# Performance work log

Measured on AMD Instinct MI355X. Metric: run time of the kernel, lower is better.

Reference implementation:

```python
import jax, jax.numpy as jnp
import numpy as np

N_NODES = 100_000
N_EDGES = 1_600_000
VOCAB = 10_000
NUM_GRAPHS = 512
D_EMB, D_HID, D_OUT = 64, 128, 64


def _sage_conv(h, src, dst, Wl, b, Wr, num_nodes):
    """PyG SAGEConv with mean aggregation: lin_l(mean_{j in N(i)} x_j) + lin_r(x_i)."""
    msgs = h[src]                                               # [E, D]
    agg = jax.ops.segment_sum(msgs, dst, num_segments=num_nodes)
    deg = jax.ops.segment_sum(jnp.ones((src.shape[0], 1), h.dtype), dst,
                              num_segments=num_nodes)
    agg = agg / jnp.maximum(deg, 1.0)                           # mean over neighbors
    return agg @ Wl + b + h @ Wr


def setup_inputs() -> dict:
    key = jax.random.key(0)
    ks = jax.random.split(key, 12)
    x = jax.random.randint(ks[0], (N_NODES,), 0, VOCAB)
    edge_index = jax.random.randint(ks[1], (2, N_EDGES), 0, N_NODES)
    batch = jnp.sort(jax.random.randint(ks[2], (N_NODES,), 0, NUM_GRAPHS))
    edge_attr = jax.random.uniform(ks[3], (N_EDGES, 1), dtype=jnp.float32)
    embed = jax.random.normal(ks[4], (VOCAB, D_EMB), dtype=jnp.float32) * 0.02
    W1l = jax.random.normal(ks[5], (D_EMB, D_HID), dtype=jnp.float32) / np.sqrt(D_EMB)
    b1 = jnp.zeros((D_HID,), jnp.float32)
    W1r = jax.random.normal(ks[6], (D_EMB, D_HID), dtype=jnp.float32) / np.sqrt(D_EMB)
    W2l = jax.random.normal(ks[7], (D_HID, D_OUT), dtype=jnp.float32) / np.sqrt(D_HID)
    b2 = jnp.zeros((D_OUT,), jnp.float32)
    W2r = jax.random.normal(ks[8], (D_HID, D_OUT), dtype=jnp.float32) / np.sqrt(D_HID)
    return {"x": x, "edge_index": edge_index, "batch": batch, "edge_attr": edge_attr,
            "embed": embed, "W1l": W1l, "b1": b1, "W1r": W1r,
            "W2l": W2l, "b2": b2, "W2r": W2r}


def reference(x, edge_index, batch, edge_attr, embed, W1l, b1, W1r, W2l, b2, W2r):
    # edge_attr is passed in the original forward but PyG SAGEConv ignores edge weights.
    src, dst = edge_index[0], edge_index[1]
    h = embed[x]                                                # [N, 64]
    h = jax.nn.relu(_sage_conv(h, src, dst, W1l, b1, W1r, N_NODES))  # [N, 128]
    h = _sage_conv(h, src, dst, W2l, b2, W2r, N_NODES)          # [N, 64]
    out = jax.ops.segment_max(h, batch, num_segments=NUM_GRAPHS)  # [G, 64]
    return out
```

## Files before the change

### kernel.cpp

```cpp
#include <hip/hip_runtime.h>
#include <cstdint>

#define NN 100000
#define NE 1600000
#define NG 512
#define NP 100032
#define VOCAB 10000
#define NBUK 64
#define BSZ 1563
#define CAP 28672
#define TILE 2048

typedef unsigned short u16;
typedef u16      u16x8  __attribute__((ext_vector_type(8)));
typedef __bf16   bf16x8 __attribute__((ext_vector_type(8)));
typedef float    f32x4  __attribute__((ext_vector_type(4)));
typedef unsigned uint4v __attribute__((ext_vector_type(4)));

__device__ __forceinline__ u16 f2bf(float f) {
    unsigned u = __float_as_uint(f);
    unsigned r = ((u >> 16) & 1u) + 0x7FFFu;
    return (u16)((u + r) >> 16);
}
__device__ __forceinline__ float bf2f(u16 h) {
    return __uint_as_float(((unsigned)h) << 16);
}

__device__ __forceinline__ unsigned encF(float f) {
    unsigned s = __float_as_uint(f);
    return (s & 0x80000000u) ? ~s : (s | 0x80000000u);
}
__device__ __forceinline__ float decF(unsigned m) {
    unsigned s = (m & 0x80000000u) ? (m ^ 0x80000000u) : ~m;
    return __uint_as_float(s);
}

template <bool HI>
__device__ __forceinline__ void gather8(const int* __restrict__ csr, int beg, int end,
                                        const u16* __restrict__ table, int lane,
                                        float acc[8]) {
    const int sub = lane >> 3, g8 = (lane & 7) * 8;
    for (int base = beg; base < end; base += 64) {
        int n = min(64, end - base);
        int s = (lane < n) ? csr[base + lane] : 0;
        for (int c = 0; c * 8 < n; c += 2) {
            int i0 = c * 8 + sub;
            int e0 = __shfl(s, i0, 64);
            int r0 = HI ? (e0 >> 17) : (e0 & 0x1FFFF);
            u16x8 v0 = *(const u16x8*)(table + (size_t)r0 * 64 + g8);
            bool m1 = (c + 1) * 8 < n;
            int i1 = (c + 1) * 8 + sub;
            int e1 = __shfl(s, m1 ? i1 : 0, 64);
            int r1 = HI ? (e1 >> 17) : (e1 & 0x1FFFF);
            u16x8 v1 = *(const u16x8*)(table + (size_t)r1 * 64 + g8);
            unsigned k0 = (i0 < n) ? 0xFFFFFFFFu : 0u;
            unsigned k1 = (m1 && i1 < n) ? 0xFFFFFFFFu : 0u;
            uint4v u0 = __builtin_bit_cast(uint4v, v0);
            uint4v u1 = __builtin_bit_cast(uint4v, v1);
            #pragma unroll
            for (int k = 0; k < 4; ++k) {
                unsigned a = u0[k] & k0, b = u1[k] & k1;
                acc[2 * k]     += __uint_as_float(a << 16);
                acc[2 * k + 1] += __uint_as_float(a & 0xFFFF0000u);
                acc[2 * k]     += __uint_as_float(b << 16);
                acc[2 * k + 1] += __uint_as_float(b & 0xFFFF0000u);
            }
        }
    }
}

__device__ __forceinline__ float reduce_dim(const float acc[8], float* sT, int lane) {
    const int sub = lane >> 3, g8 = (lane & 7) * 8;
    #pragma unroll
    for (int j = 0; j < 8; ++j) sT[sub * 64 + g8 + j] = acc[j];
    float t = 0.0f;
    #pragma unroll
    for (int sg = 0; sg < 8; ++sg) t += sT[sg * 64 + lane];
    return t;
}

__device__ __forceinline__ void prepW_body(const float* __restrict__ Wa,
                                           const float* __restrict__ Wb,
                                           int mode, u16* __restrict__ Wpk, int idx) {
    int fid = idx >> 6, lane = idx & 63;
    int cT = fid >> 2, ks = fid & 3;
    int quad = lane >> 4, l16 = lane & 15;
    int n = cT * 16 + l16;
    u16x8 v;
    #pragma unroll
    for (int j = 0; j < 8; ++j) {
        int k = ks * 32 + quad * 8 + j;
        float f = (mode == 0) ? (k < 64 ? Wa[k * 128 + n] : Wb[(k - 64) * 128 + n])
                              : (n < 64 ? Wa[k * 64 + n] : Wb[k * 64 + (n - 64)]);
        v[j] = f2bf(f);
    }
    *(u16x8*)(Wpk + idx * 8) = v;
}

__global__ __launch_bounds__(256) void k_prep(
        const float* __restrict__ emb, u16* __restrict__ embB,
        const float* __restrict__ W1l, const float* __restrict__ W1r,
        u16* __restrict__ Wpk1,
        const float* __restrict__ W2l, const float* __restrict__ W2r,
        u16* __restrict__ Wpk2, unsigned* __restrict__ om) {
    int bid = blockIdx.x, t = threadIdx.x;
    if (bid < 2500) {
        int i = bid * 256 + t;
        if (i < VOCAB * 64) embB[i] = f2bf(emb[i]);
    } else if (bid < 2508) {
        prepW_body(W1l, W1r, 0, Wpk1, (bid - 2500) * 256 + t);
    } else if (bid < 2516) {
        prepW_body(W2l, W2r, 1, Wpk2, (bid - 2508) * 256 + t);
    } else {
        int i = (bid - 2516) * 256 + t;
        if (i < NG * 64) om[i] = 0x007FFFFFu;
    }
}

__global__ __launch_bounds__(256) void k_bucket(const int* __restrict__ ei,
                                                int* __restrict__ gcur,
                                                unsigned* __restrict__ gbuf) {
    __shared__ int cnt[NBUK];
    __shared__ int start[NBUK];
    __shared__ int gbase[NBUK];
    __shared__ unsigned buf[TILE];
    __shared__ unsigned char bkt[TILE];
    const int t = threadIdx.x;
    const int e0 = blockIdx.x * (NE / 256);
    const int e1 = e0 + (NE / 256);
    for (int tb = e0; tb < e1; tb += TILE) {
        const int tc = min(TILE, e1 - tb);
        if (t < NBUK) cnt[t] = 0;
        __syncthreads();
        unsigned ent[TILE / 256];
        unsigned char eb[TILE / 256];
        u16 rk[TILE / 256];
        int nm = 0;
        for (int i = t; i < tc; i += 256) {
            int dst = ei[NE + tb + i];
            int src = ei[tb + i];
            unsigned b = (unsigned)dst / BSZ;
            unsigned dl = (unsigned)dst - b * BSZ;
            ent[nm] = (dl << 17) | (unsigned)src;
            eb[nm] = (unsigned char)b;
            rk[nm] = (u16)atomicAdd(&cnt[b], 1);
            ++nm;
        }
        __syncthreads();
        if (t < 64) {
            int c = cnt[t];
            int s = c;
            #pragma unroll
            for (int d = 1; d < 64; d <<= 1) {
                int v = __shfl_up(s, d, 64);
                if (t >= d) s += v;
            }
            start[t] = s - c;
            gbase[t] = atomicAdd(&gcur[t], c);
        }
        __syncthreads();
        for (int k = 0; k < nm; ++k) {
            int pos = start[eb[k]] + rk[k];
            buf[pos] = ent[k];
            bkt[pos] = eb[k];
        }
        __syncthreads();
        for (int i = t; i < tc; i += 256) {
            unsigned b = bkt[i];
            gbuf[(size_t)b * CAP + gbase[b] + (i - start[b])] = buf[i];
        }
        __syncthreads();
    }
}

__global__ __launch_bounds__(1024) void k_csr(const unsigned* __restrict__ gbuf,
                                              const int* __restrict__ gcur,
                                              const int* __restrict__ x,
                                              int* __restrict__ off,
                                              int* __restrict__ csr) {
    __shared__ int hist[BSZ];
    __shared__ int curL[BSZ];
    __shared__ int sc[1024];
    __shared__ int sb[64];
    const int b = blockIdx.x, t = threadIdx.x;
    for (int i = t; i < BSZ; i += 1024) hist[i] = 0;
    if (t < 64) sb[t] = (t < b) ? gcur[t] : 0;
    __syncthreads();
    const int size = gcur[b];
    const unsigned* gb = gbuf + (size_t)b * CAP;
    for (int i = t; i < size; i += 1024)
        atomicAdd(&hist[gb[i] >> 17], 1);
    for (int d = 32; d > 0; d >>= 1) {
        if (t < d) sb[t] += sb[t + d];
        __syncthreads();
    }
    const int gbase = sb[0];
    int a0 = (2 * t < BSZ) ? hist[2 * t] : 0;
    int a1 = (2 * t + 1 < BSZ) ? hist[2 * t + 1] : 0;
    sc[t] = a0 + a1;
    __syncthreads();
    for (int d = 1; d < 1024; d <<= 1) {
        int v = (t >= d) ? sc[t - d] : 0;
        __syncthreads();
        sc[t] += v;
        __syncthreads();
    }
    int ex = (t == 0) ? 0 : sc[t - 1];
    if (2 * t < BSZ) hist[2 * t] = ex;
    if (2 * t + 1 < BSZ) hist[2 * t + 1] = ex + a0;
    __syncthreads();
    const int g0 = b * BSZ;
    for (int i = t; i < BSZ; i += 1024) {
        int v = gbase + hist[i];
        curL[i] = v;
        if (g0 + i <= NN) off[g0 + i] = v;
    }
    __syncthreads();
    for (int i = t; i < size; i += 1024) {
        unsigned ent = gb[i];
        int src = (int)(ent & 0x1FFFFu);
        int dl  = (int)(ent >> 17);
        int pos = atomicAdd(&curL[dl], 1);
        csr[pos] = src | (x[src] << 17);
    }
}

__global__ __launch_bounds__(256) void k_gather1(const int* __restrict__ off,
                                                 const int* __restrict__ csr,
                                                 const int* __restrict__ x,
                                                 const u16* __restrict__ embB,
                                                 u16* __restrict__ A1) {
    __shared__ float sT[4][512];
    int wv = threadIdx.x >> 6, lane = threadIdx.x & 63;
    for (int grp = blockIdx.x; grp * 4 < NN; grp += gridDim.x) {
        int wid = grp * 4 + wv;
        int beg = off[wid], end = off[wid + 1];
        float acc[8] = {0.f, 0.f, 0.f, 0.f, 0.f, 0.f, 0.f, 0.f};
        gather8<true>(csr, beg, end, embB, lane, acc);
        float t = reduce_dim(acc, sT[wv], lane);
        A1[wid * 128 + lane] = f2bf(t / fmaxf((float)(end - beg), 1.0f));
        A1[wid * 128 + 64 + lane] = embB[x[wid] * 64 + lane];
    }
}

__global__ __launch_bounds__(256) void k_gemm12(
        const u16* __restrict__ A1, const u16* __restrict__ Wpk1,
        const u16* __restrict__ Wpk2, const float* __restrict__ b1,
        u16* __restrict__ P, u16* __restrict__ Q) {
    __shared__ __align__(16) u16 sH1[64][136];
    int w = threadIdx.x >> 6, lane = threadIdx.x & 63;
    int quad = lane >> 4, l16 = lane & 15;
    u16x8 bf1[2][4], bf2[2][4];
    #pragma unroll
    for (int ct = 0; ct < 2; ++ct)
        #pragma unroll
        for (int ks = 0; ks < 4; ++ks) {
            int fid = (w * 2 + ct) * 4 + ks;
            bf1[ct][ks] = *(const u16x8*)(Wpk1 + (fid * 64 + lane) * 8);
            bf2[ct][ks] = *(const u16x8*)(Wpk2 + (fid * 64 + lane) * 8);
        }
    int r0 = blockIdx.x * 64;
    #pragma unroll
    for (int rt = 0; rt < 4; ++rt) {
        int row = r0 + rt * 16 + l16;
        u16x8 a[4];
        #pragma unroll
        for (int ks = 0; ks < 4; ++ks)
            a[ks] = *(const u16x8*)(A1 + row * 128 + ks * 32 + quad * 8);
        #pragma unroll
        for (int ct = 0; ct < 2; ++ct) {
            f32x4 acc = {0.f, 0.f, 0.f, 0.f};
            #pragma unroll
            for (int ks = 0; ks < 4; ++ks)
                acc = __builtin_amdgcn_mfma_f32_16x16x32_bf16(
                    __builtin_bit_cast(bf16x8, a[ks]),
                    __builtin_bit_cast(bf16x8, bf1[ct][ks]), acc, 0, 0, 0);
            int col = w * 32 + ct * 16 + l16;
            float bias = b1[col];
            int lr = rt * 16 + quad * 4;
            #pragma unroll
            for (int reg = 0; reg < 4; ++reg)
                sH1[lr + reg][col] = f2bf(fmaxf(acc[reg] + bias, 0.f));
        }
    }
    __syncthreads();
    #pragma unroll
    for (int rt = 0; rt < 4; ++rt) {
        u16x8 a[4];
        #pragma unroll
        for (int ks = 0; ks < 4; ++ks)
            a[ks] = *(const u16x8*)(&sH1[rt * 16 + l16][ks * 32 + quad * 8]);
        #pragma unroll
        for (int ct = 0; ct < 2; ++ct) {
            f32x4 acc = {0.f, 0.f, 0.f, 0.f};
            #pragma unroll
            for (int ks = 0; ks < 4; ++ks)
                acc = __builtin_amdgcn_mfma_f32_16x16x32_bf16(
                    __builtin_bit_cast(bf16x8, a[ks]),
                    __builtin_bit_cast(bf16x8, bf2[ct][ks]), acc, 0, 0, 0);
            int col = w * 32 + ct * 16 + l16;
            int gr = r0 + rt * 16 + quad * 4;
            u16* dstT = (col < 64) ? P : Q;
            int c = col & 63;
            #pragma unroll
            for (int reg = 0; reg < 4; ++reg)
                dstT[(gr + reg) * 64 + c] = f2bf(acc[reg]);
        }
    }
}

__global__ __launch_bounds__(256) void k_final(const int* __restrict__ off,
                                               const int* __restrict__ csr,
                                               const u16* __restrict__ P,
                                               const u16* __restrict__ Q,
                                               const float* __restrict__ b2,
                                               const int* __restrict__ batch,
                                               unsigned* __restrict__ om) {
    __shared__ float sT[4][512];
    __shared__ float sR[4][64];
    __shared__ int sG[4];
    int wv = threadIdx.x >> 6, lane = threadIdx.x & 63;
    for (int grp = blockIdx.x; grp * 4 < NN; grp += gridDim.x) {
        int node = grp * 4 + wv;
        int beg = off[node], end = off[node + 1];
        float acc[8] = {0.f, 0.f, 0.f, 0.f, 0.f, 0.f, 0.f, 0.f};
        gather8<false>(csr, beg, end, P, lane, acc);
        float t = reduce_dim(acc, sT[wv], lane);
        float r = t / fmaxf((float)(end - beg), 1.0f) + b2[lane]
                + bf2f(Q[node * 64 + lane]);
        int g = batch[node];
        sR[wv][lane] = r;
        if (lane == 0) sG[wv] = g;
        __syncthreads();
        bool leader = (wv == 0) || (sG[wv - 1] != g);
        if (leader) {
            float m = r;
            for (int u = wv + 1; u < 4 && sG[u] == g; ++u) m = fmaxf(m, sR[u][lane]);
            atomicMax(&om[g * 64 + lane], encF(m));
        }
        __syncthreads();
    }
}

__global__ void k_decode(const unsigned* __restrict__ om, float* __restrict__ out) {
    int i = blockIdx.x * blockDim.x + threadIdx.x;
    if (i < NG * 64) out[i] = decF(om[i]);
}

extern "C" void kernel_launch(void* const* d_in, const int* in_sizes, int n_in,
                              void* d_out, int out_size, void* d_ws, size_t ws_size,
                              hipStream_t stream) {
    const int*   x     = (const int*)d_in[0];
    const int*   ei    = (const int*)d_in[1];
    const int*   batch = (const int*)d_in[2];
    const float* emb   = (const float*)d_in[4];
    const float* W1l   = (const float*)d_in[5];
    const float* b1    = (const float*)d_in[6];
    const float* W1r   = (const float*)d_in[7];
    const float* W2l   = (const float*)d_in[8];
    const float* b2    = (const float*)d_in[9];
    const float* W2r   = (const float*)d_in[10];
    float* out = (float*)d_out;

    char* p = (char*)d_ws;
    u16* A1   = (u16*)p;               p += (size_t)NP * 128 * 2;
    u16* P    = (u16*)p;               p += (size_t)NP * 64 * 2;
    u16* Q    = (u16*)p;               p += (size_t)NP * 64 * 2;
    int* csr  = (int*)p;               p += (size_t)NE * 4;
    unsigned* gbuf = (unsigned*)p;     p += (size_t)NBUK * CAP * 4;
    int* gcur = (int*)p;               p += NBUK * 4;
    int* off  = (int*)p;               p += (size_t)(NN + 1) * 4;
    u16* Wpk1 = (u16*)p;               p += 16384 * 2;
    u16* Wpk2 = (u16*)p;               p += 16384 * 2;
    u16* embB = (u16*)p;               p += (size_t)VOCAB * 64 * 2;
    unsigned* om = (unsigned*)p;

    hipMemsetAsync(gcur, 0, sizeof(int) * NBUK, stream);
    k_prep<<<2644, 256, 0, stream>>>(emb, embB, W1l, W1r, Wpk1, W2l, W2r, Wpk2, om);
    k_bucket<<<256, 256, 0, stream>>>(ei, gcur, gbuf);
    k_csr<<<NBUK, 1024, 0, stream>>>(gbuf, gcur, x, off, csr);
    k_gather1<<<2048, 256, 0, stream>>>(off, csr, x, embB, A1);
    k_gemm12<<<NP / 64, 256, 0, stream>>>(A1, Wpk1, Wpk2, b1, P, Q);
    k_final<<<2048, 256, 0, stream>>>(off, csr, P, Q, b2, batch, om);
    k_decode<<<(NG * 64 + 255) / 256, 256, 0, stream>>>(om, out);
}
```

Baseline: 253.2 us.

## Use 256 CSR buckets with wave-shuffle scans and deepen gather unroll

```diff
diff --git a/kernel.cpp b/kernel.cpp
--- a/kernel.cpp
+++ b/kernel.cpp
@@ -6,9 +6,9 @@
 #define NG 512
 #define NP 100032
 #define VOCAB 10000
-#define NBUK 64
-#define BSZ 1563
-#define CAP 28672
+#define NBUK 256
+#define BSZ 391
+#define CAP 7680
 #define TILE 2048
 
 typedef unsigned short u16;
@@ -43,27 +43,27 @@
     for (int base = beg; base < end; base += 64) {
         int n = min(64, end - base);
         int s = (lane < n) ? csr[base + lane] : 0;
-        for (int c = 0; c * 8 < n; c += 2) {
-            int i0 = c * 8 + sub;
-            int e0 = __shfl(s, i0, 64);
-            int r0 = HI ? (e0 >> 17) : (e0 & 0x1FFFF);
-            u16x8 v0 = *(const u16x8*)(table + (size_t)r0 * 64 + g8);
-            bool m1 = (c + 1) * 8 < n;
-            int i1 = (c + 1) * 8 + sub;
-            int e1 = __shfl(s, m1 ? i1 : 0, 64);
-            int r1 = HI ? (e1 >> 17) : (e1 & 0x1FFFF);
-            u16x8 v1 = *(const u16x8*)(table + (size_t)r1 * 64 + g8);
-            unsigned k0 = (i0 < n) ? 0xFFFFFFFFu : 0u;
-            unsigned k1 = (m1 && i1 < n) ? 0xFFFFFFFFu : 0u;
-            uint4v u0 = __builtin_bit_cast(uint4v, v0);
-            uint4v u1 = __builtin_bit_cast(uint4v, v1);
-            #pragma unroll
-            for (int k = 0; k < 4; ++k) {
-                unsigned a = u0[k] & k0, b = u1[k] & k1;
-                acc[2 * k]     += __uint_as_float(a << 16);
-                acc[2 * k + 1] += __uint_as_float(a & 0xFFFF0000u);
-                acc[2 * k]     += __uint_as_float(b << 16);
-                acc[2 * k + 1] += __uint_as_float(b & 0xFFFF0000u);
+        for (int c = 0; c * 8 < n; c += 4) {
+            u16x8 vv[4];
+            unsigned kk[4];
+            #pragma unroll
+            for (int u = 0; u < 4; ++u) {
+                int i = (c + u) * 8 + sub;
+                bool act = (c + u) * 8 < n;
+                int e = __shfl(s, act ? i : 0, 64);
+                int r = HI ? (e >> 17) : (e & 0x1FFFF);
+                vv[u] = *(const u16x8*)(table + (size_t)r * 64 + g8);
+                kk[u] = (act && i < n) ? 0xFFFFFFFFu : 0u;
+            }
+            #pragma unroll
+            for (int u = 0; u < 4; ++u) {
+                uint4v uv = __builtin_bit_cast(uint4v, vv[u]);
+                #pragma unroll
+                for (int k = 0; k < 4; ++k) {
+                    unsigned a = uv[k] & kk[u];
+                    acc[2 * k]     += __uint_as_float(a << 16);
+                    acc[2 * k + 1] += __uint_as_float(a & 0xFFFF0000u);
+                }
             }
         }
     }
@@ -123,6 +123,7 @@
     __shared__ int cnt[NBUK];
     __shared__ int start[NBUK];
     __shared__ int gbase[NBUK];
+    __shared__ int wsum[4];
     __shared__ unsigned buf[TILE];
     __shared__ unsigned char bkt[TILE];
     const int t = threadIdx.x;
@@ -130,7 +131,7 @@
     const int e1 = e0 + (NE / 256);
     for (int tb = e0; tb < e1; tb += TILE) {
         const int tc = min(TILE, e1 - tb);
-        if (t < NBUK) cnt[t] = 0;
+        cnt[t] = 0;
         __syncthreads();
         unsigned ent[TILE / 256];
         unsigned char eb[TILE / 256];
@@ -147,15 +148,20 @@
             ++nm;
         }
         __syncthreads();
-        if (t < 64) {
+        {
             int c = cnt[t];
             int s = c;
             #pragma unroll
             for (int d = 1; d < 64; d <<= 1) {
                 int v = __shfl_up(s, d, 64);
-                if (t >= d) s += v;
+                if ((t & 63) >= d) s += v;
             }
-            start[t] = s - c;
+            if ((t & 63) == 63) wsum[t >> 6] = s;
+            __syncthreads();
+            int pre = 0;
+            #pragma unroll
+            for (int w = 0; w < 4; ++w) pre += (w < (t >> 6)) ? wsum[w] : 0;
+            start[t] = pre + s - c;
             gbase[t] = atomicAdd(&gcur[t], c);
         }
         __syncthreads();
@@ -173,50 +179,50 @@
     }
 }
 
-__global__ __launch_bounds__(1024) void k_csr(const unsigned* __restrict__ gbuf,
-                                              const int* __restrict__ gcur,
-                                              const int* __restrict__ x,
-                                              int* __restrict__ off,
-                                              int* __restrict__ csr) {
+__global__ __launch_bounds__(512) void k_csr(const unsigned* __restrict__ gbuf,
+                                             const int* __restrict__ gcur,
+                                             const int* __restrict__ x,
+                                             int* __restrict__ off,
+                                             int* __restrict__ csr) {
     __shared__ int hist[BSZ];
     __shared__ int curL[BSZ];
-    __shared__ int sc[1024];
-    __shared__ int sb[64];
+    __shared__ int wsum[8];
+    __shared__ int sred[8];
     const int b = blockIdx.x, t = threadIdx.x;
-    for (int i = t; i < BSZ; i += 1024) hist[i] = 0;
-    if (t < 64) sb[t] = (t < b) ? gcur[t] : 0;
+    if (t < BSZ) hist[t] = 0;
     __syncthreads();
     const int size = gcur[b];
     const unsigned* gb = gbuf + (size_t)b * CAP;
-    for (int i = t; i < size; i += 1024)
+    for (int i = t; i < size; i += 512)
         atomicAdd(&hist[gb[i] >> 17], 1);
-    for (int d = 32; d > 0; d >>= 1) {
-        if (t < d) sb[t] += sb[t + d];
-        __syncthreads();
-    }
-    const int gbase = sb[0];
-    int a0 = (2 * t < BSZ) ? hist[2 * t] : 0;
-    int a1 = (2 * t + 1 < BSZ) ? hist[2 * t + 1] : 0;
-    sc[t] = a0 + a1;
-    __syncthreads();
-    for (int d = 1; d < 1024; d <<= 1) {
-        int v = (t >= d) ? sc[t - d] : 0;
-        __syncthreads();
-        sc[t] += v;
-        __syncthreads();
-    }
-    int ex = (t == 0) ? 0 : sc[t - 1];
-    if (2 * t < BSZ) hist[2 * t] = ex;
-    if (2 * t + 1 < BSZ) hist[2 * t + 1] = ex + a0;
-    __syncthreads();
-    const int g0 = b * BSZ;
-    for (int i = t; i < BSZ; i += 1024) {
-        int v = gbase + hist[i];
-        curL[i] = v;
-        if (g0 + i <= NN) off[g0 + i] = v;
-    }
-    __syncthreads();
-    for (int i = t; i < size; i += 1024) {
+    {
+        int v = (t < 256 && t < b) ? gcur[t] : 0;
+        #pragma unroll
+        for (int d = 32; d > 0; d >>= 1) v += __shfl_down(v, d, 64);
+        if ((t & 63) == 0) sred[t >> 6] = v;
+    }
+    __syncthreads();
+    const int gbase = sred[0] + sred[1] + sred[2] + sred[3];
+    int h = (t < BSZ) ? hist[t] : 0;
+    int s = h;
+    #pragma unroll
+    for (int d = 1; d < 64; d <<= 1) {
+        int v = __shfl_up(s, d, 64);
+        if ((t & 63) >= d) s += v;
+    }
+    if ((t & 63) == 63) wsum[t >> 6] = s;
+    __syncthreads();
+    int pre = 0;
+    #pragma unroll
+    for (int w = 0; w < 7; ++w) pre += (w < (t >> 6)) ? wsum[w] : 0;
+    if (t < BSZ) {
+        int ex = gbase + pre + s - h;
+        curL[t] = ex;
+        int g0 = b * BSZ;
+        if (g0 + t <= NN) off[g0 + t] = ex;
+    }
+    __syncthreads();
+    for (int i = t; i < size; i += 512) {
         unsigned ent = gb[i];
         int src = (int)(ent & 0x1FFFFu);
         int dl  = (int)(ent >> 17);
@@ -378,7 +384,7 @@
     hipMemsetAsync(gcur, 0, sizeof(int) * NBUK, stream);
     k_prep<<<2644, 256, 0, stream>>>(emb, embB, W1l, W1r, Wpk1, W2l, W2r, Wpk2, om);
     k_bucket<<<256, 256, 0, stream>>>(ei, gcur, gbuf);
-    k_csr<<<NBUK, 1024, 0, stream>>>(gbuf, gcur, x, off, csr);
+    k_csr<<<NBUK, 512, 0, stream>>>(gbuf, gcur, x, off, csr);
     k_gather1<<<2048, 256, 0, stream>>>(off, csr, x, embB, A1);
     k_gemm12<<<NP / 64, 256, 0, stream>>>(A1, Wpk1, Wpk2, b1, P, Q);
     k_final<<<2048, 256, 0, stream>>>(off, csr, P, Q, b2, batch, om);
```

Result: faster. 226.7 us (-10.5%).
